# Kernel tuning notes

Measured on AMD Instinct MI355X. Metric: run time of the kernel, lower is better.

Reference implementation:

```python
import jax, jax.numpy as jnp
import numpy as np

N_NODES = 100000
N_EDGES = 3200000
NUM_FEATURES = 256
HIDDEN = 16
NUM_CLASSES = 40


def gcn_conv(x, edge_index, W, b, num_nodes):
    """PyG GCNConv: linear -> add self-loops -> symmetric deg norm -> scatter-add -> bias."""
    x = x @ W  # [N, out]
    loop = jnp.arange(num_nodes)
    src = jnp.concatenate([edge_index[0], loop])  # messages flow src -> dst
    dst = jnp.concatenate([edge_index[1], loop])
    # degree of target nodes (with self-loops)
    deg = jax.ops.segment_sum(jnp.ones_like(dst, dtype=x.dtype), dst,
                              num_segments=num_nodes)
    dinv = jnp.where(deg > 0, jax.lax.rsqrt(deg), 0.0)
    norm = dinv[src] * dinv[dst]  # [E+N]
    out = jax.ops.segment_sum(x[src] * norm[:, None], dst,
                              num_segments=num_nodes)
    return out + b


def setup_inputs() -> dict:
    key = jax.random.key(0)
    k1, k2, k3, k4 = jax.random.split(key, 4)
    x = jax.random.normal(k1, (N_NODES, NUM_FEATURES), dtype=jnp.float32)
    edge_index = jax.random.randint(k2, (2, N_EDGES), 0, N_NODES, dtype=jnp.int64)
    W1 = jax.random.normal(k3, (NUM_FEATURES, HIDDEN), dtype=jnp.float32) / np.sqrt(NUM_FEATURES)
    b1 = jnp.zeros((HIDDEN,), dtype=jnp.float32)
    W2 = jax.random.normal(k4, (HIDDEN, NUM_CLASSES), dtype=jnp.float32) / np.sqrt(HIDDEN)
    b2 = jnp.zeros((NUM_CLASSES,), dtype=jnp.float32)
    return {"x": x, "edge_index": edge_index, "W1": W1, "b1": b1, "W2": W2, "b2": b2}


def reference(x, edge_index, W1, b1, W2, b2):
    h = jax.nn.relu(gcn_conv(x, edge_index, W1, b1, N_NODES))
    return gcn_conv(h, edge_index, W2, b2, N_NODES)
```

## Files before the change

kernel.cpp:

```cpp
#include <hip/hip_runtime.h>
#include <hip/hip_fp16.h>

#define N_NODES   100000
#define N_EDGES   3200000
#define F_IN      256
#define HID       16
#define NCLS      40

#define CHUNK     8192
#define NBLK      ((N_EDGES + CHUNK - 1) / CHUNK)
#define B2SHIFT   9
#define NB2       ((N_NODES + 511) >> B2SHIFT)
#define BCAP      17408

#define COMP(v, kk) ((kk) == 0 ? (v).x : (kk) == 1 ? (v).y : (kk) == 2 ? (v).z : (v).w)

__global__ __launch_bounds__(256) void k1_hist_gemm(const int* __restrict__ ei,
                                                    const float* __restrict__ x,
                                                    const float* __restrict__ W1,
                                                    int* __restrict__ hist_blk,
                                                    __half* __restrict__ y1h) {
    __shared__ int h[NB2];
    int blk = blockIdx.x, t = threadIdx.x;

    for (int i = t; i < NB2; i += 256) h[i] = 0;
    __syncthreads();
    int e0 = blk * CHUNK;
    int eN = min(CHUNK, N_EDGES - e0);
    const int4* d4 = (const int4*)(ei + N_EDGES + e0);
    for (int i = t; i < (eN >> 2); i += 256) {
        int4 d = d4[i];
        atomicAdd(&h[d.x >> B2SHIFT], 1);
        atomicAdd(&h[d.y >> B2SHIFT], 1);
        atomicAdd(&h[d.z >> B2SHIFT], 1);
        atomicAdd(&h[d.w >> B2SHIFT], 1);
    }
    __syncthreads();
    for (int i = t; i < NB2; i += 256) hist_blk[i * NBLK + blk] = h[i];

    int n = blk * 256 + t;
    if (n >= N_NODES) return;

    const float4* xr = (const float4*)(x + (size_t)n * F_IN);
    float acc[HID];
    #pragma unroll
    for (int j = 0; j < HID; j++) acc[j] = 0.f;

    #pragma unroll 4
    for (int k4 = 0; k4 < F_IN / 4; k4++) {
        float4 xv = xr[k4];
        #pragma unroll
        for (int kk = 0; kk < 4; kk++) {
            const float xs = COMP(xv, kk);
            const float* w = W1 + (k4 * 4 + kk) * HID;
            #pragma unroll
            for (int hh = 0; hh < HID; hh++) acc[hh] += xs * w[hh];
        }
    }
    __half2 hp[8];
    #pragma unroll
    for (int j = 0; j < 8; j++)
        hp[j] = __float22half2_rn(make_float2(acc[2 * j], acc[2 * j + 1]));
    float4* o = (float4*)(y1h + (size_t)n * HID);
    o[0] = ((float4*)hp)[0];
    o[1] = ((float4*)hp)[1];
}

__global__ __launch_bounds__(512) void k2_bin(const int* __restrict__ ei,
                                              const int* __restrict__ hist_blk,
                                              int* __restrict__ buf) {
    __shared__ int cur[NB2];
    __shared__ int sc[256];
    int blk = blockIdx.x, t = threadIdx.x;
    int pre = 0, tot = 0;
    if (t < NB2) {
        const int* row = hist_blk + t * NBLK;
        for (int k = 0; k < NBLK; k++) {
            int v = row[k];
            pre += (k < blk) ? v : 0;
            tot += v;
        }
    }
    if (t < 256) sc[t] = tot;
    __syncthreads();
    for (int off = 1; off < 256; off <<= 1) {
        int u = 0;
        if (t < 256 && t >= off) u = sc[t - off];
        __syncthreads();
        if (t < 256) sc[t] += u;
        __syncthreads();
    }
    if (t < NB2) cur[t] = (sc[t] - tot) + pre;
    __syncthreads();

    int e0 = blk * CHUNK;
    int eN = min(CHUNK, N_EDGES - e0);
    const int4* s4 = (const int4*)(ei + e0);
    const int4* d4 = (const int4*)(ei + N_EDGES + e0);
    for (int i = t; i < (eN >> 2); i += 512) {
        int4 d = d4[i], s = s4[i];
        int p0 = atomicAdd(&cur[d.x >> B2SHIFT], 1); buf[p0] = ((d.x & 511) << 17) | s.x;
        int p1 = atomicAdd(&cur[d.y >> B2SHIFT], 1); buf[p1] = ((d.y & 511) << 17) | s.y;
        int p2 = atomicAdd(&cur[d.z >> B2SHIFT], 1); buf[p2] = ((d.z & 511) << 17) | s.z;
        int p3 = atomicAdd(&cur[d.w >> B2SHIFT], 1); buf[p3] = ((d.w & 511) << 17) | s.w;
    }
}

__global__ __launch_bounds__(512) void k3_build(const int* __restrict__ buf,
                                               const int* __restrict__ hist_blk,
                                               int* __restrict__ rowptr,
                                               float* __restrict__ dinv,
                                               int* __restrict__ csr_src,
                                               __half* __restrict__ y1h) {
    __shared__ int lbuf[BCAP];
    __shared__ int hist[512], offs[512], cur[512];
    __shared__ int sc[256];
    __shared__ int s_base, s_cnt;
    int b = blockIdx.x, t = threadIdx.x;

    int tot = 0;
    if (t < NB2) {
        const int* row = hist_blk + t * NBLK;
        for (int k = 0; k < NBLK; k++) tot += row[k];
    }
    if (t < 256) sc[t] = tot;
    hist[t] = 0;
    __syncthreads();
    for (int off = 1; off < 256; off <<= 1) {
        int u = 0;
        if (t < 256 && t >= off) u = sc[t - off];
        __syncthreads();
        if (t < 256) sc[t] += u;
        __syncthreads();
    }
    if (t == b) { s_base = sc[b] - tot; s_cnt = tot; }
    __syncthreads();
    int base = s_base, cnt = s_cnt;

    for (int i = t; i < cnt; i += 512) {
        int v = buf[base + i];
        if (i < BCAP) lbuf[i] = v;
        atomicAdd(&hist[v >> 17], 1);
    }
    __syncthreads();
    int v = hist[t];
    offs[t] = v;
    __syncthreads();
    for (int off = 1; off < 512; off <<= 1) {
        int u = (t >= off) ? offs[t - off] : 0;
        __syncthreads();
        offs[t] += u;
        __syncthreads();
    }
    int ex = offs[t] - v;
    int n = (b << B2SHIFT) + t;
    if (n < N_NODES) {
        rowptr[n] = base + ex;
        float dv = rsqrtf((float)(v + 1));
        dinv[n] = dv;
        float4* yr = (float4*)(y1h + (size_t)n * HID);
        float4 a = yr[0], bq = yr[1];
        __half2* ah = (__half2*)&a;
        __half2* bh = (__half2*)&bq;
        #pragma unroll
        for (int j = 0; j < 4; j++) {
            float2 fa = __half22float2(ah[j]);
            float2 fb = __half22float2(bh[j]);
            ah[j] = __float22half2_rn(make_float2(fa.x * dv, fa.y * dv));
            bh[j] = __float22half2_rn(make_float2(fb.x * dv, fb.y * dv));
        }
        yr[0] = a;
        yr[1] = bq;
    }
    if (b == 0 && t == 0) rowptr[N_NODES] = N_EDGES;
    cur[t] = ex;
    __syncthreads();
    for (int i = t; i < cnt; i += 512) {
        int p = (i < BCAP) ? lbuf[i] : buf[base + i];
        int pos = atomicAdd(&cur[p >> 17], 1);
        csr_src[base + pos] = p & 0x1FFFF;
    }
}

__device__ __forceinline__ void acc_row(const float4* __restrict__ tab, int s, float* acc) {
    float4 v0 = tab[(size_t)s * 2 + 0];
    float4 v1 = tab[(size_t)s * 2 + 1];
    const __half2* a0 = (const __half2*)&v0;
    const __half2* a1 = (const __half2*)&v1;
    #pragma unroll
    for (int j = 0; j < 4; j++) {
        float2 f0 = __half22float2(a0[j]);
        float2 f1 = __half22float2(a1[j]);
        acc[2 * j]         += f0.x;
        acc[2 * j + 1]     += f0.y;
        acc[8 + 2 * j]     += f1.x;
        acc[8 + 2 * j + 1] += f1.y;
    }
}

__device__ __forceinline__ void acc_row2(const float4* __restrict__ tab, int s0, int s1, float* acc) {
    float4 v0 = tab[(size_t)s0 * 2 + 0];
    float4 v1 = tab[(size_t)s0 * 2 + 1];
    float4 v2 = tab[(size_t)s1 * 2 + 0];
    float4 v3 = tab[(size_t)s1 * 2 + 1];
    const __half2* a0 = (const __half2*)&v0;
    const __half2* a1 = (const __half2*)&v1;
    const __half2* b0 = (const __half2*)&v2;
    const __half2* b1 = (const __half2*)&v3;
    #pragma unroll
    for (int j = 0; j < 4; j++) {
        float2 f0 = __half22float2(a0[j]);
        float2 f1 = __half22float2(a1[j]);
        float2 g0 = __half22float2(b0[j]);
        float2 g1 = __half22float2(b1[j]);
        acc[2 * j]         += f0.x + g0.x;
        acc[2 * j + 1]     += f0.y + g0.y;
        acc[8 + 2 * j]     += f1.x + g1.x;
        acc[8 + 2 * j + 1] += f1.y + g1.y;
    }
}

__global__ __launch_bounds__(256) void gather1_kernel(const int* __restrict__ rowptr,
                                                      const int* __restrict__ csr_src,
                                                      const __half* __restrict__ y1h,
                                                      const float* __restrict__ b1,
                                                      const float* __restrict__ dinv,
                                                      __half* __restrict__ zh) {
    int n   = blockIdx.x * 64 + (threadIdx.x >> 2);
    int sub = threadIdx.x & 3;
    if (n >= N_NODES) return;
    const float4* tab = (const float4*)y1h;
    int beg = rowptr[n], end = rowptr[n + 1];
    float acc[16];
    #pragma unroll
    for (int i = 0; i < 16; i++) acc[i] = 0.f;
    if (sub == 0) acc_row(tab, n, acc);
    int e = beg + sub;
    for (; e + 4 < end; e += 8)
        acc_row2(tab, csr_src[e], csr_src[e + 4], acc);
    if (e < end) acc_row(tab, csr_src[e], acc);
    #pragma unroll
    for (int m = 1; m < 4; m <<= 1) {
        #pragma unroll
        for (int i = 0; i < 16; i++) acc[i] += __shfl_xor(acc[i], m, 4);
    }
    if (sub < 2) {
        float dvn = dinv[n];
        const float4* b1q = (const float4*)b1;
        float4 ba = b1q[sub * 2], bb = b1q[sub * 2 + 1];
        float bv[8] = {ba.x, ba.y, ba.z, ba.w, bb.x, bb.y, bb.z, bb.w};
        __half2 outp[4];
        #pragma unroll
        for (int j = 0; j < 4; j++) {
            float2 r;
            r.x = fmaxf(dvn * acc[sub * 8 + 2 * j]     + bv[2 * j],     0.f) * dvn;
            r.y = fmaxf(dvn * acc[sub * 8 + 2 * j + 1] + bv[2 * j + 1], 0.f) * dvn;
            outp[j] = __float22half2_rn(r);
        }
        *(float4*)(zh + (size_t)n * HID + sub * 8) = *(float4*)outp;
    }
}

__global__ __launch_bounds__(256) void gather2_kernel(const int* __restrict__ rowptr,
                                                      const int* __restrict__ csr_src,
                                                      const __half* __restrict__ zh,
                                                      const float* __restrict__ W2,
                                                      const float* __restrict__ b2,
                                                      const float* __restrict__ dinv,
                                                      float* __restrict__ out) {
    __shared__ float W2s[HID * NCLS];
    __shared__ float b2s[NCLS];
    int t = threadIdx.x;
    for (int i = t; i < HID * NCLS; i += 256) W2s[i] = W2[i];
    if (t < NCLS) b2s[t] = b2[t];
    __syncthreads();

    int n   = blockIdx.x * 64 + (t >> 2);
    int sub = t & 3;
    if (n >= N_NODES) return;
    const float4* tab = (const float4*)zh;
    int beg = rowptr[n], end = rowptr[n + 1];
    float acc[16];
    #pragma unroll
    for (int i = 0; i < 16; i++) acc[i] = 0.f;
    if (sub == 0) acc_row(tab, n, acc);
    int e = beg + sub;
    for (; e + 4 < end; e += 8)
        acc_row2(tab, csr_src[e], csr_src[e + 4], acc);
    if (e < end) acc_row(tab, csr_src[e], acc);
    #pragma unroll
    for (int m = 1; m < 4; m <<= 1) {
        #pragma unroll
        for (int i = 0; i < 16; i++) acc[i] += __shfl_xor(acc[i], m, 4);
    }
    float dv = dinv[n];
    int c0 = sub * 10;
    float o[10];
    #pragma unroll
    for (int j = 0; j < 10; j++) o[j] = 0.f;
    #pragma unroll
    for (int h = 0; h < HID; h++) {
        float a = acc[h];
        const float* w = &W2s[h * NCLS + c0];
        #pragma unroll
        for (int j = 0; j < 10; j++) o[j] += a * w[j];
    }
    float* op = out + (size_t)n * NCLS + c0;
    #pragma unroll
    for (int j = 0; j < 5; j++) {
        float2 r = make_float2(dv * o[2 * j]     + b2s[c0 + 2 * j],
                               dv * o[2 * j + 1] + b2s[c0 + 2 * j + 1]);
        *(float2*)(op + 2 * j) = r;
    }
}

extern "C" void kernel_launch(void* const* d_in, const int* in_sizes, int n_in,
                              void* d_out, int out_size, void* d_ws, size_t ws_size,
                              hipStream_t stream) {
    const float* x   = (const float*)d_in[0];
    const int*   ei  = (const int*)  d_in[1];
    const float* W1  = (const float*)d_in[2];
    const float* b1  = (const float*)d_in[3];
    const float* W2  = (const float*)d_in[4];
    const float* b2  = (const float*)d_in[5];
    float* out = (float*)d_out;

    char* ws = (char*)d_ws;
    size_t off = 0;
    int*   hist_blk = (int*)(ws + off); off += (size_t)NB2 * NBLK * 4;
    off = (off + 15) & ~(size_t)15;
    int*    rowptr  = (int*)   (ws + off); off += (size_t)(N_NODES + 1) * 4;
    off = (off + 15) & ~(size_t)15;
    float*  dinv    = (float*) (ws + off); off += (size_t)N_NODES * 4;
    int*    csr_src = (int*)   (ws + off); off += (size_t)N_EDGES * 4;
    int*    buf     = (int*)   (ws + off); off += (size_t)N_EDGES * 4;
    __half* y1h     = (__half*)(ws + off); off += (size_t)N_NODES * HID * 2;
    __half* zh      = (__half*)(ws + off); off += (size_t)N_NODES * HID * 2;

    k1_hist_gemm <<<NBLK, 256, 0, stream>>>(ei, x, W1, hist_blk, y1h);
    k2_bin       <<<NBLK, 512, 0, stream>>>(ei, hist_blk, buf);
    k3_build     <<<NB2, 512, 0, stream>>>(buf, hist_blk, rowptr, dinv, csr_src, y1h);
    gather1_kernel<<<(N_NODES + 63) / 64, 256, 0, stream>>>(rowptr, csr_src, y1h, b1, dinv, zh);
    gather2_kernel<<<(N_NODES + 63) / 64, 256, 0, stream>>>(rowptr, csr_src, zh, W2, b2, dinv, out);
}
```

Measured before the change: 331.0 us.

## Split-K the first-layer GEMM across waves and decouple it from histogram blocks

The fused histogram+GEMM kernel now launches one block per 64 nodes instead of one per 256 nodes. Each of the four waves computes a quarter of the 256-wide dot product, and the partial sums are reduced through shared memory before the fp16 store. Only the first NBLK blocks do the edge histogram, and the edge chunk size is doubled, which halves the number of histogram partitions that the binning kernel scans. The goal is more memory-level parallelism on the 100 MB x read. The cost is an extra LDS reduction and barrier, plus coarser edge chunks in the binning stage.

```diff
diff --git a/kernel.cpp b/kernel.cpp
--- a/kernel.cpp
+++ b/kernel.cpp
@@ -7,11 +7,12 @@
 #define HID       16
 #define NCLS      40
 
-#define CHUNK     8192
+#define CHUNK     16384
 #define NBLK      ((N_EDGES + CHUNK - 1) / CHUNK)
 #define B2SHIFT   9
 #define NB2       ((N_NODES + 511) >> B2SHIFT)
 #define BCAP      17408
+#define G1BLKS    ((N_NODES + 63) / 64)
 
 #define COMP(v, kk) ((kk) == 0 ? (v).x : (kk) == 1 ? (v).y : (kk) == 2 ? (v).z : (v).w)
 
@@ -20,50 +21,74 @@
                                                     const float* __restrict__ W1,
                                                     int* __restrict__ hist_blk,
                                                     __half* __restrict__ y1h) {
-    __shared__ int h[NB2];
+    __shared__ float4 part[4 * 64 * 4];
+    int* h = (int*)part;
     int blk = blockIdx.x, t = threadIdx.x;
 
-    for (int i = t; i < NB2; i += 256) h[i] = 0;
-    __syncthreads();
-    int e0 = blk * CHUNK;
-    int eN = min(CHUNK, N_EDGES - e0);
-    const int4* d4 = (const int4*)(ei + N_EDGES + e0);
-    for (int i = t; i < (eN >> 2); i += 256) {
-        int4 d = d4[i];
-        atomicAdd(&h[d.x >> B2SHIFT], 1);
-        atomicAdd(&h[d.y >> B2SHIFT], 1);
-        atomicAdd(&h[d.z >> B2SHIFT], 1);
-        atomicAdd(&h[d.w >> B2SHIFT], 1);
-    }
-    __syncthreads();
-    for (int i = t; i < NB2; i += 256) hist_blk[i * NBLK + blk] = h[i];
-
-    int n = blk * 256 + t;
-    if (n >= N_NODES) return;
-
-    const float4* xr = (const float4*)(x + (size_t)n * F_IN);
+    if (blk < NBLK) {
+        for (int i = t; i < NB2; i += 256) h[i] = 0;
+        __syncthreads();
+        int e0 = blk * CHUNK;
+        int eN = min(CHUNK, N_EDGES - e0);
+        const int4* d4 = (const int4*)(ei + N_EDGES + e0);
+        for (int i = t; i < (eN >> 2); i += 256) {
+            int4 d = d4[i];
+            atomicAdd(&h[d.x >> B2SHIFT], 1);
+            atomicAdd(&h[d.y >> B2SHIFT], 1);
+            atomicAdd(&h[d.z >> B2SHIFT], 1);
+            atomicAdd(&h[d.w >> B2SHIFT], 1);
+        }
+        __syncthreads();
+        for (int i = t; i < NB2; i += 256) hist_blk[i * NBLK + blk] = h[i];
+        __syncthreads();
+    }
+
+    int nl = t & 63;
+    int n  = blk * 64 + nl;
+    int wv = __builtin_amdgcn_readfirstlane(t >> 6);
+    int nc = min(n, N_NODES - 1);
+
+    const float4* xr = (const float4*)(x + (size_t)nc * F_IN) + wv * 16;
+    const float*  w  = W1 + wv * 64 * HID;
+
     float acc[HID];
     #pragma unroll
     for (int j = 0; j < HID; j++) acc[j] = 0.f;
 
     #pragma unroll 4
-    for (int k4 = 0; k4 < F_IN / 4; k4++) {
+    for (int k4 = 0; k4 < 16; k4++) {
         float4 xv = xr[k4];
         #pragma unroll
         for (int kk = 0; kk < 4; kk++) {
             const float xs = COMP(xv, kk);
-            const float* w = W1 + (k4 * 4 + kk) * HID;
+            const float* wr = w + (k4 * 4 + kk) * HID;
             #pragma unroll
-            for (int hh = 0; hh < HID; hh++) acc[hh] += xs * w[hh];
-        }
-    }
-    __half2 hp[8];
-    #pragma unroll
-    for (int j = 0; j < 8; j++)
-        hp[j] = __float22half2_rn(make_float2(acc[2 * j], acc[2 * j + 1]));
-    float4* o = (float4*)(y1h + (size_t)n * HID);
-    o[0] = ((float4*)hp)[0];
-    o[1] = ((float4*)hp)[1];
+            for (int hh = 0; hh < HID; hh++) acc[hh] += xs * wr[hh];
+        }
+    }
+    float4* pw = &part[(wv * 64 + nl) * 4];
+    pw[0] = make_float4(acc[ 0], acc[ 1], acc[ 2], acc[ 3]);
+    pw[1] = make_float4(acc[ 4], acc[ 5], acc[ 6], acc[ 7]);
+    pw[2] = make_float4(acc[ 8], acc[ 9], acc[10], acc[11]);
+    pw[3] = make_float4(acc[12], acc[13], acc[14], acc[15]);
+    __syncthreads();
+
+    int rn = t >> 2, q = t & 3;
+    float4 s0 = part[(0 * 64 + rn) * 4 + q];
+    float4 s1 = part[(1 * 64 + rn) * 4 + q];
+    float4 s2 = part[(2 * 64 + rn) * 4 + q];
+    float4 s3 = part[(3 * 64 + rn) * 4 + q];
+    float4 s = make_float4(s0.x + s1.x + s2.x + s3.x,
+                           s0.y + s1.y + s2.y + s3.y,
+                           s0.z + s1.z + s2.z + s3.z,
+                           s0.w + s1.w + s2.w + s3.w);
+    int gn = blk * 64 + rn;
+    if (gn < N_NODES) {
+        float2 r;
+        ((__half2*)&r)[0] = __float22half2_rn(make_float2(s.x, s.y));
+        ((__half2*)&r)[1] = __float22half2_rn(make_float2(s.z, s.w));
+        *(float2*)(y1h + (size_t)gn * HID + q * 4) = r;
+    }
 }
 
 __global__ __launch_bounds__(512) void k2_bin(const int* __restrict__ ei,
@@ -337,7 +362,7 @@
     __half* y1h     = (__half*)(ws + off); off += (size_t)N_NODES * HID * 2;
     __half* zh      = (__half*)(ws + off); off += (size_t)N_NODES * HID * 2;
 
-    k1_hist_gemm <<<NBLK, 256, 0, stream>>>(ei, x, W1, hist_blk, y1h);
+    k1_hist_gemm <<<G1BLKS, 256, 0, stream>>>(ei, x, W1, hist_blk, y1h);
     k2_bin       <<<NBLK, 512, 0, stream>>>(ei, hist_blk, buf);
     k3_build     <<<NB2, 512, 0, stream>>>(buf, hist_blk, rowptr, dinv, csr_src, y1h);
     gather1_kernel<<<(N_NODES + 63) / 64, 256, 0, stream>>>(rowptr, csr_src, y1h, b1, dinv, zh);
```

New measurement: 317.4 us. 1.04x faster.
